# Performance work log

Measured on AMD Instinct MI355X. Metric: run time of the kernel, lower is better.

The kernel has to match this reference:

```python
import jax, jax.numpy as jnp
import numpy as np

N_NODES = 50000
N_EDGES = 800000
IN_FEATS = 256
N_HEADS = 4
OUT_FEATS = 32
NEG_SLOPE = 0.2


def setup_inputs() -> dict:
    key = jax.random.key(0)
    k_feat, k_src, k_dst, k_fc, k_al, k_ar, k_res = jax.random.split(key, 7)
    feat = jax.random.normal(k_feat, (N_NODES, IN_FEATS), dtype=jnp.float32)
    src = jax.random.randint(k_src, (N_EDGES,), 0, N_NODES)
    dst = jax.random.randint(k_dst, (N_EDGES,), 0, N_NODES)
    # xavier-normal-ish scales
    s_fc = (2.0 / (IN_FEATS + N_HEADS * OUT_FEATS)) ** 0.5
    W_fc = jax.random.normal(k_fc, (N_HEADS * OUT_FEATS, IN_FEATS), dtype=jnp.float32) * s_fc
    s_a = (2.0 / (1 + N_HEADS * OUT_FEATS)) ** 0.5
    attn_l = jax.random.normal(k_al, (N_HEADS, OUT_FEATS), dtype=jnp.float32) * s_a
    attn_r = jax.random.normal(k_ar, (N_HEADS, OUT_FEATS), dtype=jnp.float32) * s_a
    W_res = jax.random.normal(k_res, (N_HEADS * OUT_FEATS, IN_FEATS), dtype=jnp.float32) * s_fc
    return {"feat": feat, "src": src, "dst": dst, "W_fc": W_fc,
            "attn_l": attn_l, "attn_r": attn_r, "W_res": W_res}


def reference(feat, src, dst, W_fc, attn_l, attn_r, W_res):
    N = feat.shape[0]
    H, D = attn_l.shape
    ones_e = jnp.ones(src.shape[0], dtype=feat.dtype)

    # projection: [N, H, D]
    h = (feat @ W_fc.T).reshape(N, H, D)
    feat_dst = h  # dst features are pre-norm (torch code aliases before * norm)

    # symmetric norm on source side: out_degree^-0.5
    out_deg = jax.ops.segment_sum(ones_e, src, num_segments=N)
    feat_src = h * (jnp.clip(out_deg, 1.0) ** -0.5)[:, None, None]

    # per-node attention halves -> per-edge score, leaky relu
    el = jnp.einsum('nhd,hd->nh', feat_src, attn_l)  # [N, H]
    er = jnp.einsum('nhd,hd->nh', feat_dst, attn_r)  # [N, H]
    e = jax.nn.leaky_relu(el[src] + er[dst], NEG_SLOPE)  # [E, H]

    # edge_softmax over incoming edges of each dst node
    emax = jax.ops.segment_max(e, dst, num_segments=N)
    emax = jnp.where(jnp.isfinite(emax), emax, 0.0)  # guard empty segments
    ex = jnp.exp(e - emax[dst])
    denom = jax.ops.segment_sum(ex, dst, num_segments=N)
    a = ex / denom[dst]  # [E, H]

    # weighted scatter-sum of messages: u_mul_e + sum
    msg = feat_src[src] * a[:, :, None]  # [E, H, D]
    rst = jax.ops.segment_sum(msg, dst, num_segments=N)  # [N, H, D]

    # symmetric norm on destination side: in_degree^0.5
    in_deg = jax.ops.segment_sum(ones_e, dst, num_segments=N)
    rst = rst * jnp.sqrt(jnp.clip(in_deg, 1.0))[:, None, None]

    # residual projection
    rst = rst + (feat @ W_res.T).reshape(N, H, D)
    return rst
```

## Files before the change

### kernel.cpp

```cpp
#include <hip/hip_runtime.h>
#include <hip/hip_bf16.h>
#include <math.h>

#define HD 128
#define IN_F 256
#define NEG_SLOPE 0.2f
#define NMAX 50000
#define GB 512

typedef __attribute__((ext_vector_type(8))) short short8;
typedef __attribute__((ext_vector_type(4))) float f32x4;

__device__ __forceinline__ unsigned short f2bf(float x) {
    __hip_bfloat16 b = __float2bfloat16(x);
    return *(unsigned short*)&b;
}
__device__ __forceinline__ float bf2f(unsigned short u) {
    unsigned int v = ((unsigned int)u) << 16;
    float f;
    __builtin_memcpy(&f, &v, 4);
    return f;
}
__device__ __forceinline__ short8 pack8(float4 f0, float4 f1) {
    short8 v;
    v[0] = (short)f2bf(f0.x); v[1] = (short)f2bf(f0.y);
    v[2] = (short)f2bf(f0.z); v[3] = (short)f2bf(f0.w);
    v[4] = (short)f2bf(f1.x); v[5] = (short)f2bf(f1.y);
    v[6] = (short)f2bf(f1.z); v[7] = (short)f2bf(f1.w);
    return v;
}

__global__ void cvt_w_kernel(const float4* __restrict__ wfc, const float4* __restrict__ wres,
                             ushort4* __restrict__ w16, int n4each) {
    int idx = blockIdx.x * blockDim.x + threadIdx.x;
    if (idx >= 2 * n4each) return;
    float4 f = (idx < n4each) ? wfc[idx] : wres[idx - n4each];
    ushort4 u;
    u.x = f2bf(f.x); u.y = f2bf(f.y); u.z = f2bf(f.z); u.w = f2bf(f.w);
    w16[idx] = u;
}

__global__ __launch_bounds__(256) void ew_kernel(const float* __restrict__ wfc,
                                                 const float* __restrict__ attn_l,
                                                 const float* __restrict__ attn_r,
                                                 unsigned short* __restrict__ ew16) {
    int h = blockIdx.x;
    int k = threadIdx.x;
    float sl = 0.f, sr = 0.f;
#pragma unroll 8
    for (int d = 0; d < 32; d++) {
        float w = wfc[(size_t)(h * 32 + d) * IN_F + k];
        sl += attn_l[h * 32 + d] * w;
        sr += attn_r[h * 32 + d] * w;
    }
    ew16[h * IN_F + k] = f2bf(sl);
    ew16[(4 + h) * IN_F + k] = f2bf(sr);
    ew16[(8 + h) * IN_F + k] = 0;
    ew16[(12 + h) * IN_F + k] = 0;
}

__global__ __launch_bounds__(512) void hist_kernel(const int* __restrict__ src,
                                                   const int* __restrict__ dst,
                                                   unsigned short* __restrict__ pc_src,
                                                   unsigned short* __restrict__ pc_dst,
                                                   int N, int E, int chunk) {
    __shared__ unsigned int h[NMAX / 2];
    int tid = threadIdx.x;
    int nh = N >> 1;
    uint4* h4 = (uint4*)h;
    for (int i = tid; i < (nh >> 2); i += 512) h4[i] = make_uint4(0, 0, 0, 0);
    for (int i = (nh & ~3) + tid; i < nh; i += 512) h[i] = 0;
    __syncthreads();

    const int* arr = blockIdx.y ? src : dst;
    int e1 = min(E, (int)(blockIdx.x + 1) * chunk);
    for (int e = blockIdx.x * chunk + tid; e < e1; e += 512) {
        int v = arr[e];
        atomicAdd(&h[v >> 1], 1u << ((v & 1) << 4));
    }
    __syncthreads();

    unsigned short* pc = (blockIdx.y ? pc_src : pc_dst) + (size_t)blockIdx.x * N;
    uint4* pc4 = (uint4*)pc;
    for (int i = tid; i < (nh >> 2); i += 512) pc4[i] = h4[i];
    for (int i = (nh & ~3) + tid; i < nh; i += 512) ((unsigned int*)pc)[i] = h[i];
}

__global__ __launch_bounds__(256) void sum_scan1_kernel(
    const unsigned short* __restrict__ pc_src, unsigned short* __restrict__ pc_dst,
    int* __restrict__ out_cnt, int* __restrict__ deg, int* __restrict__ bsum,
    int N, int C) {
    __shared__ int wsum[4];
    int n = blockIdx.x * 256 + threadIdx.x;
    int sd = 0;
    if (n < N) {
        int ss = 0;
        for (int c = 0; c < C; c++) {
            ss += pc_src[(size_t)c * N + n];
            unsigned short v = pc_dst[(size_t)c * N + n];
            pc_dst[(size_t)c * N + n] = (unsigned short)sd;
            sd += v;
        }
        out_cnt[n] = ss;
        deg[n] = sd;
    }
    int v = (n < N) ? sd : 0;
#pragma unroll
    for (int d = 1; d < 64; d <<= 1) v += __shfl_xor(v, d);
    if ((threadIdx.x & 63) == 0) wsum[threadIdx.x >> 6] = v;
    __syncthreads();
    if (threadIdx.x == 0) bsum[blockIdx.x] = wsum[0] + wsum[1] + wsum[2] + wsum[3];
}

__global__ __launch_bounds__(256) void scan2_kernel(int* __restrict__ bsum, int nb,
                                                    int* __restrict__ row_start_N, int E) {
    __shared__ int wtot[4];
    int tid = threadIdx.x, lane = tid & 63, wid = tid >> 6;
    int v = (tid < nb) ? bsum[tid] : 0;
    int incl = v;
#pragma unroll
    for (int d = 1; d < 64; d <<= 1) {
        int t = __shfl_up(incl, d);
        if (lane >= d) incl += t;
    }
    if (lane == 63) wtot[wid] = incl;
    __syncthreads();
    int woff = 0;
    for (int w = 0; w < wid; w++) woff += wtot[w];
    if (tid < nb) bsum[tid] = woff + incl - v;
    if (tid == 0) *row_start_N = E;
}

__global__ __launch_bounds__(256) void scan3_kernel(const int* __restrict__ deg,
                                                    const int* __restrict__ boff,
                                                    int* __restrict__ row_start, int N) {
    __shared__ int wsum[4];
    int i = blockIdx.x * 256 + threadIdx.x;
    int lane = threadIdx.x & 63, wid = threadIdx.x >> 6;
    int v = (i < N) ? deg[i] : 0;
    int incl = v;
#pragma unroll
    for (int d = 1; d < 64; d <<= 1) {
        int t = __shfl_up(incl, d);
        if (lane >= d) incl += t;
    }
    if (lane == 63) wsum[wid] = incl;
    __syncthreads();
    int woff = 0;
    for (int w = 0; w < wid; w++) woff += wsum[w];
    int excl = boff[blockIdx.x] + woff + incl - v;
    if (i < N) row_start[i] = excl;
}

__global__ __launch_bounds__(512) void place_kernel(const int* __restrict__ src,
                                                    const int* __restrict__ dst,
                                                    const unsigned short* __restrict__ chunkpre,
                                                    const int* __restrict__ row_start,
                                                    int* __restrict__ esrc,
                                                    int N, int E, int chunk) {
    __shared__ unsigned int cur[NMAX / 2];
    int tid = threadIdx.x;
    int nh = N >> 1;
    const unsigned short* cp = chunkpre + (size_t)blockIdx.x * N;
    const uint4* cp4 = (const uint4*)cp;
    uint4* cur4 = (uint4*)cur;
    for (int i = tid; i < (nh >> 2); i += 512) cur4[i] = cp4[i];
    for (int i = (nh & ~3) + tid; i < nh; i += 512) cur[i] = ((const unsigned int*)cp)[i];
    __syncthreads();

    int e1 = min(E, (int)(blockIdx.x + 1) * chunk);
    for (int e = blockIdx.x * chunk + tid; e < e1; e += 512) {
        int d = dst[e], s = src[e];
        int sh = (d & 1) << 4;
        unsigned int old = atomicAdd(&cur[d >> 1], 1u << sh);
        int rank = (old >> sh) & 0xffff;
        esrc[row_start[d] + rank] = s;
    }
}

__global__ __launch_bounds__(256, 2) void gemm_fused(
    const float* __restrict__ feat, const __hip_bfloat16* __restrict__ w16,
    const __hip_bfloat16* __restrict__ ew16, const int* __restrict__ out_cnt,
    unsigned short* __restrict__ h16, unsigned short* __restrict__ resid16,
    float* __restrict__ el, float* __restrict__ er, int N, int ntiles) {
    __shared__ unsigned short sA[2][32 * 256];
    int tid = threadIdx.x;
    int lane = tid & 63, wn = tid >> 6;
    int l15 = lane & 15, lg = lane >> 4;
    int colbase = wn * 64;
    bool w0 = (wn == 0);
    bool isH = (wn < 2);
    int colloc = colbase & 127;

    short8 breg[4][8];
#pragma unroll
    for (int ni = 0; ni < 4; ni++) {
        const __hip_bfloat16* bp = w16 + (size_t)(colbase + ni * 16 + l15) * IN_F + lg * 8;
#pragma unroll
        for (int kk = 0; kk < 8; kk++) breg[ni][kk] = *(const short8*)(bp + kk * 32);
    }
    short8 ereg[8];
    {
        const __hip_bfloat16* ep = ew16 + (size_t)l15 * IN_F + lg * 8;
#pragma unroll
        for (int kk = 0; kk < 8; kk++) ereg[kk] = *(const short8*)(ep + kk * 32);
    }

    int srow[4], sgc[4];
#pragma unroll
    for (int i = 0; i < 4; i++) {
        int G = i * 256 + tid;
        srow[i] = G >> 5;
        sgc[i] = G & 31;
    }

    float4 fA[4][2];
    int t = blockIdx.x;
#pragma unroll
    for (int i = 0; i < 4; i++) {
        int gm = t * 32 + srow[i];
        gm = (gm < N) ? gm : (N - 1);
        const float4* fp = (const float4*)(feat + (size_t)gm * IN_F + sgc[i] * 8);
        fA[i][0] = fp[0];
        fA[i][1] = fp[1];
    }
#pragma unroll
    for (int i = 0; i < 4; i++)
        *(short8*)&sA[0][srow[i] * 256 + ((sgc[i] ^ (srow[i] & 7)) * 8)] =
            pack8(fA[i][0], fA[i][1]);

    int cur = 0;
    for (; t < ntiles; t += GB) {
        __syncthreads();

        int tn = t + GB;
        if (tn < ntiles) {
#pragma unroll
            for (int i = 0; i < 4; i++) {
                int gm = tn * 32 + srow[i];
                gm = (gm < N) ? gm : (N - 1);
                const float4* fp = (const float4*)(feat + (size_t)gm * IN_F + sgc[i] * 8);
                fA[i][0] = fp[0];
                fA[i][1] = fp[1];
            }
        }

        f32x4 acc[2][4], accE[2];
#pragma unroll
        for (int i = 0; i < 2; i++) {
            accE[i] = (f32x4){0.f, 0.f, 0.f, 0.f};
#pragma unroll
            for (int j = 0; j < 4; j++) acc[i][j] = (f32x4){0.f, 0.f, 0.f, 0.f};
        }
#pragma unroll
        for (int kk = 0; kk < 8; kk++) {
            short8 a[2];
#pragma unroll
            for (int mi = 0; mi < 2; mi++) {
                int row = mi * 16 + l15;
                int gs = (kk * 4 + lg) ^ (row & 7);
                a[mi] = *(const short8*)&sA[cur][row * 256 + gs * 8];
            }
#pragma unroll
            for (int mi = 0; mi < 2; mi++)
#pragma unroll
                for (int ni = 0; ni < 4; ni++)
                    acc[mi][ni] = __builtin_amdgcn_mfma_f32_16x16x32_bf16(
                        a[mi], breg[ni][kk], acc[mi][ni], 0, 0, 0);
            if (w0) {
#pragma unroll
                for (int mi = 0; mi < 2; mi++)
                    accE[mi] = __builtin_amdgcn_mfma_f32_16x16x32_bf16(
                        a[mi], ereg[kk], accE[mi], 0, 0, 0);
            }
        }

        int bm = t * 32;
#pragma unroll
        for (int mi = 0; mi < 2; mi++) {
#pragma unroll
            for (int reg = 0; reg < 4; reg++) {
                int r = bm + mi * 16 + lg * 4 + reg;
                bool valid = (r < N);
                int rr = valid ? r : 0;
                if (isH) {
                    float nrm = rsqrtf(fmaxf((float)out_cnt[rr], 1.0f));
                    if (valid) {
#pragma unroll
                        for (int ni = 0; ni < 4; ni++)
                            h16[(size_t)r * HD + colloc + ni * 16 + l15] =
                                f2bf(acc[mi][ni][reg] * nrm);
                        if (w0) {
                            float ev = accE[mi][reg];
                            if (l15 < 4) el[r * 4 + l15] = ev * nrm;
                            else if (l15 < 8) er[r * 4 + (l15 - 4)] = ev;
                        }
                    }
                } else if (valid) {
#pragma unroll
                    for (int ni = 0; ni < 4; ni++)
                        resid16[(size_t)r * HD + colloc + ni * 16 + l15] =
                            f2bf(acc[mi][ni][reg]);
                }
            }
        }

        if (tn < ntiles) {
#pragma unroll
            for (int i = 0; i < 4; i++)
                *(short8*)&sA[cur ^ 1][srow[i] * 256 + ((sgc[i] ^ (srow[i] & 7)) * 8)] =
                    pack8(fA[i][0], fA[i][1]);
        }
        cur ^= 1;
    }
}

__global__ __launch_bounds__(256) void agg_kernel(const unsigned short* __restrict__ h16,
                                                  const float* __restrict__ el,
                                                  const float* __restrict__ er,
                                                  const int* __restrict__ row_start,
                                                  const int* __restrict__ esrc,
                                                  const unsigned short* __restrict__ resid16,
                                                  float* __restrict__ out, int N) {
    int wid = threadIdx.x >> 6, lane = threadIdx.x & 63;
    int n = blockIdx.x * 4 + wid;
    if (n >= N) return;
    int es = lane >> 4;
    int l15 = lane & 15;
    int h = l15 >> 2;
    int d0 = l15 * 8;
    int beg = row_start[n], end = row_start[n + 1];
    float erh = er[n * 4 + h];
    float den = 0.f;
    float acc[8];
#pragma unroll
    for (int j = 0; j < 8; j++) acc[j] = 0.f;

    if (beg < end) {
        bool ok0, ok1;
        float ev0, ev1; short8 hv0, hv1;
        {
            int i0 = beg + es, i1 = beg + 4 + es;
            ok0 = i0 < end; ok1 = i1 < end;
            int s0 = esrc[ok0 ? i0 : beg];
            int s1 = esrc[ok1 ? i1 : beg];
            ev0 = el[s0 * 4 + h]; ev1 = el[s1 * 4 + h];
            hv0 = *(const short8*)(h16 + (size_t)s0 * HD + d0);
            hv1 = *(const short8*)(h16 + (size_t)s1 * HD + d0);
        }
        for (int base = beg + 8; base < end; base += 8) {
            int i0 = base + es, i1 = base + 4 + es;
            bool p0 = i0 < end, p1 = i1 < end;
            int t0 = esrc[p0 ? i0 : beg];
            int t1 = esrc[p1 ? i1 : beg];
            float fv0 = el[t0 * 4 + h];
            float fv1 = el[t1 * 4 + h];
            short8 g0 = *(const short8*)(h16 + (size_t)t0 * HD + d0);
            short8 g1 = *(const short8*)(h16 + (size_t)t1 * HD + d0);
            float e0 = ev0 + erh; e0 = (e0 > 0.f) ? e0 : NEG_SLOPE * e0;
            float e1 = ev1 + erh; e1 = (e1 > 0.f) ? e1 : NEG_SLOPE * e1;
            float ex0 = ok0 ? __expf(e0) : 0.f;
            float ex1 = ok1 ? __expf(e1) : 0.f;
            den += ex0 + ex1;
#pragma unroll
            for (int j = 0; j < 8; j++)
                acc[j] += ex0 * bf2f((unsigned short)hv0[j]) +
                          ex1 * bf2f((unsigned short)hv1[j]);
            ok0 = p0; ok1 = p1; ev0 = fv0; ev1 = fv1; hv0 = g0; hv1 = g1;
        }
        float e0 = ev0 + erh; e0 = (e0 > 0.f) ? e0 : NEG_SLOPE * e0;
        float e1 = ev1 + erh; e1 = (e1 > 0.f) ? e1 : NEG_SLOPE * e1;
        float ex0 = ok0 ? __expf(e0) : 0.f;
        float ex1 = ok1 ? __expf(e1) : 0.f;
        den += ex0 + ex1;
#pragma unroll
        for (int j = 0; j < 8; j++)
            acc[j] += ex0 * bf2f((unsigned short)hv0[j]) +
                      ex1 * bf2f((unsigned short)hv1[j]);
    }

#pragma unroll
    for (int m = 16; m < 64; m <<= 1) {
        den += __shfl_xor(den, m);
#pragma unroll
        for (int j = 0; j < 8; j++) acc[j] += __shfl_xor(acc[j], m);
    }

    if (es == 0) {
        const unsigned short* rp = resid16 + (size_t)n * HD + d0;
        short8 rv = *(const short8*)rp;
        int indeg = end - beg;
        float sc = (indeg > 0) ? sqrtf((float)indeg) / den : 0.f;
        float o[8];
#pragma unroll
        for (int j = 0; j < 8; j++)
            o[j] = sc * acc[j] + bf2f((unsigned short)rv[j]);
        float* op = out + (size_t)n * HD + d0;
        *(float4*)op = make_float4(o[0], o[1], o[2], o[3]);
        *(float4*)(op + 4) = make_float4(o[4], o[5], o[6], o[7]);
    }
}

extern "C" void kernel_launch(void* const* d_in, const int* in_sizes, int n_in,
                              void* d_out, int out_size, void* d_ws, size_t ws_size,
                              hipStream_t stream) {
    const float* feat   = (const float*)d_in[0];
    const int*   src    = (const int*)d_in[1];
    const int*   dst    = (const int*)d_in[2];
    const float* W_fc   = (const float*)d_in[3];
    const float* attn_l = (const float*)d_in[4];
    const float* attn_r = (const float*)d_in[5];
    const float* W_res  = (const float*)d_in[6];
    float* out = (float*)d_out;

    int N = in_sizes[0] / IN_F;
    int E = in_sizes[1];
    int nb = (N + 255) / 256;

    size_t off = 0;
    auto alloc = [&](size_t bytes) {
        size_t o = off;
        off = (off + bytes + 255) & ~(size_t)255;
        return o;
    };
    char* ws = (char*)d_ws;
    unsigned short* h16     = (unsigned short*)(ws + alloc((size_t)N * HD * 2));
    unsigned short* resid16 = (unsigned short*)(ws + alloc((size_t)N * HD * 2));
    __hip_bfloat16* w16     = (__hip_bfloat16*)(ws + alloc((size_t)2 * HD * IN_F * 2));
    unsigned short* ew16    = (unsigned short*)(ws + alloc((size_t)16 * IN_F * 2));
    float* el               = (float*)(ws + alloc((size_t)N * 4 * 4));
    float* er               = (float*)(ws + alloc((size_t)N * 4 * 4));
    int* out_cnt            = (int*)(ws + alloc((size_t)N * 4));
    int* deg                = (int*)(ws + alloc((size_t)N * 4));
    int* row_start          = (int*)(ws + alloc((size_t)(N + 1) * 4));
    int* bsum               = (int*)(ws + alloc((size_t)nb * 4));
    int* esrc               = (int*)(ws + alloc((size_t)E * 4));

    size_t per_chunk = (size_t)4 * N;
    size_t avail = (ws_size > off + 4096) ? (ws_size - off - 4096) : 0;
    int C = (int)(avail / per_chunk);
    if (C > 128) C = 128;
    if (C < 32) C = 32;
    unsigned short* pc_dst = (unsigned short*)(ws + alloc((size_t)C * N * 2));
    unsigned short* pc_src = (unsigned short*)(ws + alloc((size_t)C * N * 2));
    int chunk = (E + C - 1) / C;

    int n4each = HD * IN_F / 4;
    cvt_w_kernel<<<(2 * n4each + 255) / 256, 256, 0, stream>>>(
        (const float4*)W_fc, (const float4*)W_res, (ushort4*)w16, n4each);
    ew_kernel<<<4, 256, 0, stream>>>(W_fc, attn_l, attn_r, ew16);

    hist_kernel<<<dim3(C, 2), 512, 0, stream>>>(src, dst, pc_src, pc_dst, N, E, chunk);
    sum_scan1_kernel<<<nb, 256, 0, stream>>>(pc_src, pc_dst, out_cnt, deg, bsum, N, C);
    scan2_kernel<<<1, 256, 0, stream>>>(bsum, nb, row_start + N, E);
    scan3_kernel<<<nb, 256, 0, stream>>>(deg, bsum, row_start, N);
    place_kernel<<<C, 512, 0, stream>>>(src, dst, pc_dst, row_start, esrc, N, E, chunk);

    int ntiles = (N + 31) / 32;
    gemm_fused<<<GB, 256, 0, stream>>>(feat, (const __hip_bfloat16*)w16,
                                       (const __hip_bfloat16*)ew16, out_cnt,
                                       h16, resid16, el, er, N, ntiles);

    int nb4 = (N + 3) / 4;
    agg_kernel<<<nb4, 256, 0, stream>>>(h16, el, er, row_start, esrc, resid16, out, N);
}
```

Before: 153.9 us.

## Stage GEMM weights in LDS and use 512-thread persistent blocks

The fused projection GEMM now loads the full 256x256 bf16 weight matrix into LDS (128 KB) once per block instead of holding per-wave slices in registers. Blocks grow to 8 waves, each computing 32 columns, and the grid shrinks to 256 persistent blocks. The double-buffered A tile is replaced by a single buffer with an extra barrier per tile. This lowers register pressure and the redundant weight fetch per block, at the cost of B-operand LDS reads every k-step, a large LDS footprint limiting occupancy to one block per CU, and less overlap between global loads and compute.

```diff
diff --git a/kernel.cpp b/kernel.cpp
--- a/kernel.cpp
+++ b/kernel.cpp
@@ -6,7 +6,7 @@
 #define IN_F 256
 #define NEG_SLOPE 0.2f
 #define NMAX 50000
-#define GB 512
+#define GGRID 256
 
 typedef __attribute__((ext_vector_type(8))) short short8;
 typedef __attribute__((ext_vector_type(4))) float f32x4;
@@ -178,65 +178,66 @@
     }
 }
 
-__global__ __launch_bounds__(256, 2) void gemm_fused(
+__global__ __launch_bounds__(512, 1) void gemm_fused(
     const float* __restrict__ feat, const __hip_bfloat16* __restrict__ w16,
     const __hip_bfloat16* __restrict__ ew16, const int* __restrict__ out_cnt,
     unsigned short* __restrict__ h16, unsigned short* __restrict__ resid16,
     float* __restrict__ el, float* __restrict__ er, int N, int ntiles) {
-    __shared__ unsigned short sA[2][32 * 256];
+    __shared__ unsigned short sB[256 * 256];
+    __shared__ unsigned short sA[32 * 256];
     int tid = threadIdx.x;
-    int lane = tid & 63, wn = tid >> 6;
+    int lane = tid & 63, w = tid >> 6;
     int l15 = lane & 15, lg = lane >> 4;
-    int colbase = wn * 64;
-    bool w0 = (wn == 0);
-    bool isH = (wn < 2);
-    int colloc = colbase & 127;
-
-    short8 breg[4][8];
-#pragma unroll
-    for (int ni = 0; ni < 4; ni++) {
-        const __hip_bfloat16* bp = w16 + (size_t)(colbase + ni * 16 + l15) * IN_F + lg * 8;
-#pragma unroll
-        for (int kk = 0; kk < 8; kk++) breg[ni][kk] = *(const short8*)(bp + kk * 32);
+    int c0 = w * 32;
+    bool w0 = (w == 0);
+    bool isH = (w < 4);
+    int colloc = c0 & 127;
+
+#pragma unroll
+    for (int it = 0; it < 16; ++it) {
+        int idx = it * 512 + tid;
+        int c = idx >> 5, g = idx & 31;
+        short8 v = *(const short8*)(w16 + (size_t)c * IN_F + g * 8);
+        *(short8*)&sB[c * 256 + ((g ^ (c & 7)) * 8)] = v;
     }
     short8 ereg[8];
-    {
+    if (w0) {
         const __hip_bfloat16* ep = ew16 + (size_t)l15 * IN_F + lg * 8;
 #pragma unroll
         for (int kk = 0; kk < 8; kk++) ereg[kk] = *(const short8*)(ep + kk * 32);
     }
 
-    int srow[4], sgc[4];
-#pragma unroll
-    for (int i = 0; i < 4; i++) {
-        int G = i * 256 + tid;
-        srow[i] = G >> 5;
-        sgc[i] = G & 31;
-    }
-
-    float4 fA[4][2];
+    int srow[2], sgc[2];
+#pragma unroll
+    for (int i = 0; i < 2; i++) {
+        int idx = i * 512 + tid;
+        srow[i] = idx >> 5;
+        sgc[i] = idx & 31;
+    }
+
+    float4 fA[2][2];
     int t = blockIdx.x;
 #pragma unroll
-    for (int i = 0; i < 4; i++) {
+    for (int i = 0; i < 2; i++) {
         int gm = t * 32 + srow[i];
         gm = (gm < N) ? gm : (N - 1);
         const float4* fp = (const float4*)(feat + (size_t)gm * IN_F + sgc[i] * 8);
         fA[i][0] = fp[0];
         fA[i][1] = fp[1];
     }
-#pragma unroll
-    for (int i = 0; i < 4; i++)
-        *(short8*)&sA[0][srow[i] * 256 + ((sgc[i] ^ (srow[i] & 7)) * 8)] =
-            pack8(fA[i][0], fA[i][1]);
-
-    int cur = 0;
-    for (; t < ntiles; t += GB) {
+
+    for (; t < ntiles; t += GGRID) {
         __syncthreads();
-
-        int tn = t + GB;
+#pragma unroll
+        for (int i = 0; i < 2; i++)
+            *(short8*)&sA[srow[i] * 256 + ((sgc[i] ^ (srow[i] & 7)) * 8)] =
+                pack8(fA[i][0], fA[i][1]);
+        __syncthreads();
+
+        int tn = t + GGRID;
         if (tn < ntiles) {
 #pragma unroll
-            for (int i = 0; i < 4; i++) {
+            for (int i = 0; i < 2; i++) {
                 int gm = tn * 32 + srow[i];
                 gm = (gm < N) ? gm : (N - 1);
                 const float4* fp = (const float4*)(feat + (size_t)gm * IN_F + sgc[i] * 8);
@@ -245,28 +246,34 @@
             }
         }
 
-        f32x4 acc[2][4], accE[2];
+        f32x4 acc[2][2], accE[2];
 #pragma unroll
         for (int i = 0; i < 2; i++) {
             accE[i] = (f32x4){0.f, 0.f, 0.f, 0.f};
 #pragma unroll
-            for (int j = 0; j < 4; j++) acc[i][j] = (f32x4){0.f, 0.f, 0.f, 0.f};
+            for (int j = 0; j < 2; j++) acc[i][j] = (f32x4){0.f, 0.f, 0.f, 0.f};
         }
 #pragma unroll
         for (int kk = 0; kk < 8; kk++) {
-            short8 a[2];
+            short8 a[2], b[2];
 #pragma unroll
             for (int mi = 0; mi < 2; mi++) {
                 int row = mi * 16 + l15;
                 int gs = (kk * 4 + lg) ^ (row & 7);
-                a[mi] = *(const short8*)&sA[cur][row * 256 + gs * 8];
+                a[mi] = *(const short8*)&sA[row * 256 + gs * 8];
             }
 #pragma unroll
+            for (int ni = 0; ni < 2; ni++) {
+                int c = c0 + ni * 16 + l15;
+                int gsb = (kk * 4 + lg) ^ (c & 7);
+                b[ni] = *(const short8*)&sB[c * 256 + gsb * 8];
+            }
+#pragma unroll
             for (int mi = 0; mi < 2; mi++)
 #pragma unroll
-                for (int ni = 0; ni < 4; ni++)
+                for (int ni = 0; ni < 2; ni++)
                     acc[mi][ni] = __builtin_amdgcn_mfma_f32_16x16x32_bf16(
-                        a[mi], breg[ni][kk], acc[mi][ni], 0, 0, 0);
+                        a[mi], b[ni], acc[mi][ni], 0, 0, 0);
             if (w0) {
 #pragma unroll
                 for (int mi = 0; mi < 2; mi++)
@@ -287,7 +294,7 @@
                     float nrm = rsqrtf(fmaxf((float)out_cnt[rr], 1.0f));
                     if (valid) {
 #pragma unroll
-                        for (int ni = 0; ni < 4; ni++)
+                        for (int ni = 0; ni < 2; ni++)
                             h16[(size_t)r * HD + colloc + ni * 16 + l15] =
                                 f2bf(acc[mi][ni][reg] * nrm);
                         if (w0) {
@@ -298,20 +305,12 @@
                     }
                 } else if (valid) {
 #pragma unroll
-                    for (int ni = 0; ni < 4; ni++)
+                    for (int ni = 0; ni < 2; ni++)
                         resid16[(size_t)r * HD + colloc + ni * 16 + l15] =
                             f2bf(acc[mi][ni][reg]);
                 }
             }
         }
-
-        if (tn < ntiles) {
-#pragma unroll
-            for (int i = 0; i < 4; i++)
-                *(short8*)&sA[cur ^ 1][srow[i] * 256 + ((sgc[i] ^ (srow[i] & 7)) * 8)] =
-                    pack8(fA[i][0], fA[i][1]);
-        }
-        cur ^= 1;
     }
 }
 
@@ -457,9 +456,9 @@
     place_kernel<<<C, 512, 0, stream>>>(src, dst, pc_dst, row_start, esrc, N, E, chunk);
 
     int ntiles = (N + 31) / 32;
-    gemm_fused<<<GB, 256, 0, stream>>>(feat, (const __hip_bfloat16*)w16,
-                                       (const __hip_bfloat16*)ew16, out_cnt,
-                                       h16, resid16, el, er, N, ntiles);
+    gemm_fused<<<GGRID, 512, 0, stream>>>(feat, (const __hip_bfloat16*)w16,
+                                          (const __hip_bfloat16*)ew16, out_cnt,
+                                          h16, resid16, el, er, N, ntiles);
 
     int nb4 = (N + 3) / 4;
     agg_kernel<<<nb4, 256, 0, stream>>>(h16, el, er, row_start, esrc, resid16, out, N);
```

Measured after the change: 144.5 us. 6.1% less time.
